# Kernel optimization log

Hardware: AMD Instinct MI355X
Metric: run time of the kernel (lower is better)

The kernel has to match this reference:

```python
import jax, jax.numpy as jnp
import numpy as np

N_NODES = 100000
IN_F = 128
H_F = 128
LOOKBACK = 3
N_EDGES = 640000


def setup_inputs() -> dict:
    key = jax.random.key(0)
    ks = jax.random.split(key, 16)
    s = lambda k, shp: jax.random.normal(k, shp, dtype=jnp.float32) * 0.05
    inp = {
        "feat": jax.random.normal(ks[0], (N_NODES, IN_F), dtype=jnp.float32),
        "edges": jax.random.randint(ks[1], (LOOKBACK, 2, N_EDGES), 0, N_NODES, dtype=jnp.int32),
        # conv1 (SAGEConv pool, in->h) params
        "Wp1": s(ks[2], (IN_F, IN_F)), "bp1": jnp.zeros((IN_F,), jnp.float32),
        "Ws1": s(ks[3], (H_F, IN_F)), "Wn1": s(ks[4], (H_F, IN_F)), "b1": jnp.zeros((H_F,), jnp.float32),
        # BatchNorm1d affine params (training-mode batch stats)
        "gamma": jnp.ones((H_F,), jnp.float32), "beta": jnp.zeros((H_F,), jnp.float32),
        # conv2 (SAGEConv pool, h->h) params
        "Wp2": s(ks[5], (H_F, H_F)), "bp2": jnp.zeros((H_F,), jnp.float32),
        "Ws2": s(ks[6], (H_F, H_F)), "Wn2": s(ks[7], (H_F, H_F)), "b2": jnp.zeros((H_F,), jnp.float32),
    }
    return inp


def _sage_pool_conv(h, src, dst, Wp, bp, Ws, Wn, b):
    # pool aggregator: m = relu(fc_pool(h)); neigh = max over in-edges
    m = jax.nn.relu(h @ Wp.T + bp)                      # [N, d]
    agg = jax.ops.segment_max(m[src], dst, num_segments=N_NODES)  # [N, d]
    agg = jnp.where(jnp.isfinite(agg), agg, 0.0)        # nodes with no in-edges -> 0
    return h @ Ws.T + agg @ Wn.T + b


def _batchnorm(x, gamma, beta, eps=1e-5):
    mu = jnp.mean(x, axis=0)
    var = jnp.var(x, axis=0)
    return (x - mu) * jax.lax.rsqrt(var + eps) * gamma + beta


def reference(feat, edges, Wp1, bp1, Ws1, Wn1, b1, gamma, beta, Wp2, bp2, Ws2, Wn2, b2):
    def per_graph(e):
        src, dst = e[0], e[1]
        h = _sage_pool_conv(feat, src, dst, Wp1, bp1, Ws1, Wn1, b1)
        h = _batchnorm(h, gamma, beta)
        h = jax.nn.relu(h)
        h = _sage_pool_conv(h, src, dst, Wp2, bp2, Ws2, Wn2, b2)
        return h

    return jax.vmap(per_graph)(edges)  # [lookback, N, H_F]
```

## Files before the change

### kernel.cpp

```cpp
#include <hip/hip_runtime.h>
#include <hip/hip_bf16.h>

#define NNODES 100000
#define FD 128
#define NEDGES 640000
#define NB 391
#define NT64 1563
#define GX_TWOA 170
#define GX_ONEW 340
#define GX_HEAD 512
#define OFFS_U32 100032

typedef __bf16 bf16x8 __attribute__((ext_vector_type(8)));
typedef __bf16 bf16x4 __attribute__((ext_vector_type(4)));
typedef float f32x4 __attribute__((ext_vector_type(4)));
typedef unsigned short u16x8 __attribute__((ext_vector_type(8)));

__device__ __forceinline__ bf16x8 cvt8(float4 a, float4 b) {
  bf16x8 r;
  r[0] = (__bf16)a.x; r[1] = (__bf16)a.y; r[2] = (__bf16)a.z; r[3] = (__bf16)a.w;
  r[4] = (__bf16)b.x; r[5] = (__bf16)b.y; r[6] = (__bf16)b.z; r[7] = (__bf16)b.w;
  return r;
}

__device__ __forceinline__ void gl16(const void* g, void* l) {
  __builtin_amdgcn_global_load_lds(
      (const __attribute__((address_space(1))) unsigned int*)g,
      (__attribute__((address_space(3))) unsigned int*)l, 16, 0, 0);
}

__device__ __forceinline__ void stage_abf(const __bf16* A, long row0, int M,
                                          char* l, int wid, int lane) {
  long row = row0 + lane;
  if (row > M - 1) row = M - 1;
  const char* base = (const char*)(A + row * FD);
#pragma unroll
  for (int i = 0; i < 2; ++i) {
    const int s = wid * 2 + i;
    gl16(base + s * 16, l + s * 1024);
  }
}

__device__ __forceinline__ void stage_a32(const float* A, long row0, int M,
                                          char* l, int wid, int lane) {
  long row = row0 + lane;
  if (row > M - 1) row = M - 1;
  const char* base = (const char*)(A + row * FD);
#pragma unroll
  for (int i = 0; i < 4; ++i) {
    const int s = wid * 4 + i;
    gl16(base + s * 16, l + s * 1024);
  }
}

__global__ __launch_bounds__(256) void packw6_k(
    const float* __restrict__ W0, const float* __restrict__ W1,
    const float* __restrict__ W2, const float* __restrict__ W3,
    const float* __restrict__ W4, const float* __restrict__ W5,
    __bf16* __restrict__ out) {
  const int gidx = blockIdx.x * 256 + threadIdx.x;
  const int wi = gidx >> 11;
  const int f = gidx & 2047;
  const float* W = wi == 0 ? W0 : wi == 1 ? W1 : wi == 2 ? W2
                 : wi == 3 ? W3 : wi == 4 ? W4 : W5;
  const int c = f >> 8, kk = (f >> 6) & 3, lane = f & 63;
  const int lr = lane & 15, lg = lane >> 4;
  const float* p = W + (c * 16 + lr) * FD + kk * 32 + lg * 8;
  *(bf16x8*)(out + (long)gidx * 8) = cvt8(*(const float4*)p, *(const float4*)(p + 4));
}

template <int AM>
__device__ __forceinline__ void lds_arow(const char* l, int rl, int lg,
                                         const float* __restrict__ scsh,
                                         bf16x8 (&af)[4]) {
#pragma unroll
  for (int kk = 0; kk < 4; ++kk) {
    if constexpr (AM == 0) {
      const int s = kk * 8 + lg * 2;
      const float4 x = *(const float4*)(l + s * 1024 + rl * 16);
      const float4 y = *(const float4*)(l + (s + 1) * 1024 + rl * 16);
      af[kk] = cvt8(x, y);
    } else {
      const bf16x8 r = *(const bf16x8*)(l + (kk * 4 + lg) * 1024 + rl * 16);
      if constexpr (AM == 3) {
        const int k = lg * 8 + kk * 32;
        const float4 scx = *(const float4*)(scsh + k);
        const float4 scy = *(const float4*)(scsh + k + 4);
        const float4 shx = *(const float4*)(scsh + 128 + k);
        const float4 shy = *(const float4*)(scsh + 128 + k + 4);
        bf16x8 o;
        o[0] = (__bf16)fmaxf((float)r[0] * scx.x + shx.x, 0.f);
        o[1] = (__bf16)fmaxf((float)r[1] * scx.y + shx.y, 0.f);
        o[2] = (__bf16)fmaxf((float)r[2] * scx.z + shx.z, 0.f);
        o[3] = (__bf16)fmaxf((float)r[3] * scx.w + shx.w, 0.f);
        o[4] = (__bf16)fmaxf((float)r[4] * scy.x + shy.x, 0.f);
        o[5] = (__bf16)fmaxf((float)r[5] * scy.y + shy.y, 0.f);
        o[6] = (__bf16)fmaxf((float)r[6] * scy.z + shy.z, 0.f);
        o[7] = (__bf16)fmaxf((float)r[7] * scy.w + shy.w, 0.f);
        af[kk] = o;
      } else {
        af[kk] = r;
      }
    }
  }
}

template <int A0M, int A1M, bool TWOA, bool RELU, bool OUTBF16, bool STATS, bool WRITEB>
__global__ __launch_bounds__(512, 2) void gemm_k(
    const void* __restrict__ A0, long a0s, const void* __restrict__ A1, long a1s,
    const __bf16* __restrict__ W0p, const __bf16* __restrict__ W1p,
    const float* __restrict__ bias, const float* __restrict__ scsh0,
    void* __restrict__ outp, long os, float* __restrict__ pblk,
    __bf16* __restrict__ bcopy, int M) {
  constexpr int ASZ = (A0M == 0) ? 32768 : 16384;
  constexpr int A1SZ = TWOA ? 16384 : 0;
  constexpr int LSZ = 2 * (ASZ + A1SZ) + (STATS ? 2048 : 0);
  __shared__ __align__(16) char lds[LSZ];
  char* lA0a = lds;
  char* lA1a = lds + ASZ;
  char* lA0b = lds + ASZ + A1SZ;
  char* lA1b = lds + 2 * ASZ + A1SZ;
  float* s_red = (float*)(lds + 2 * (ASZ + A1SZ));

  const int g = blockIdx.y;
  const int tid = threadIdx.x;
  const int wid = tid >> 6;
  const int lane = tid & 63;
  const int rw = wid & 1;
  const int cw = wid >> 1;
  const int lr = lane & 15;
  const int lg = lane >> 4;
  const int S = gridDim.x;

  const void* A0g = (const char*)A0 + (long)g * a0s;
  const void* A1g = (const char*)A1 + (TWOA ? (long)g * a1s : 0);
  void* outg = (char*)outp + (long)g * os;
  const float* scshg = (A0M == 3 || A1M == 3) ? scsh0 + (long)g * 256 : nullptr;

  bf16x8 bw0[2][4], bw1[2][4];
#pragma unroll
  for (int ci = 0; ci < 2; ++ci)
#pragma unroll
    for (int kk = 0; kk < 4; ++kk) {
      const long f = ((long)((cw * 2 + ci) * 4 + kk) * 64 + lane) * 8;
      bw0[ci][kk] = *(const bf16x8*)(W0p + f);
      if constexpr (TWOA) bw1[ci][kk] = *(const bf16x8*)(W1p + f);
    }

  float ps[2][4], pss[2][4];
  if constexpr (STATS) {
#pragma unroll
    for (int ci = 0; ci < 2; ++ci)
#pragma unroll
      for (int j = 0; j < 4; ++j) { ps[ci][j] = 0.f; pss[ci][j] = 0.f; }
  }

  auto stageA = [&](long t, char* la0, char* la1) {
    if constexpr (A0M == 0) stage_a32((const float*)A0g, t * 64, M, la0, wid, lane);
    else stage_abf((const __bf16*)A0g, t * 64, M, la0, wid, lane);
    if constexpr (TWOA) stage_abf((const __bf16*)A1g, t * 64, M, la1, wid, lane);
  };

  auto body = [&](long t, long tn, char* la0, char* la1, char* na0, char* na1) {
    if (tn < NT64) stageA(tn, na0, na1);

    bf16x8 a0f[2][4];
#pragma unroll
    for (int tt = 0; tt < 2; ++tt)
      lds_arow<A0M>(la0, rw * 32 + tt * 16 + lr, lg, scshg, a0f[tt]);
    bf16x8 a1f[2][4];
    if constexpr (TWOA) {
#pragma unroll
      for (int tt = 0; tt < 2; ++tt)
        lds_arow<A1M>(la1, rw * 32 + tt * 16 + lr, lg, scshg, a1f[tt]);
    }

    if constexpr (WRITEB) {
      if (cw == 0) {
#pragma unroll
        for (int tt = 0; tt < 2; ++tt) {
          const long row = t * 64 + rw * 32 + tt * 16 + lr;
          if (row < M)
#pragma unroll
            for (int kk = 0; kk < 4; ++kk)
              *(bf16x8*)(bcopy + row * FD + lg * 8 + kk * 32) = a0f[tt][kk];
        }
      }
    }

    f32x4 acc[2][2];
#pragma unroll
    for (int tt = 0; tt < 2; ++tt)
#pragma unroll
      for (int ci = 0; ci < 2; ++ci) acc[tt][ci] = (f32x4){0.f, 0.f, 0.f, 0.f};

#pragma unroll
    for (int ci = 0; ci < 2; ++ci)
#pragma unroll
      for (int tt = 0; tt < 2; ++tt)
#pragma unroll
        for (int kk = 0; kk < 4; ++kk)
          acc[tt][ci] = __builtin_amdgcn_mfma_f32_16x16x32_bf16(bw0[ci][kk], a0f[tt][kk], acc[tt][ci], 0, 0, 0);
    if constexpr (TWOA) {
#pragma unroll
      for (int ci = 0; ci < 2; ++ci)
#pragma unroll
        for (int tt = 0; tt < 2; ++tt)
#pragma unroll
          for (int kk = 0; kk < 4; ++kk)
            acc[tt][ci] = __builtin_amdgcn_mfma_f32_16x16x32_bf16(bw1[ci][kk], a1f[tt][kk], acc[tt][ci], 0, 0, 0);
    }

#pragma unroll
    for (int tt = 0; tt < 2; ++tt) {
      const long row = t * 64 + rw * 32 + tt * 16 + lr;
      const bool ok = row < M;
#pragma unroll
      for (int ci = 0; ci < 2; ++ci) {
        const int cb = cw * 32 + ci * 16 + lg * 4;
        f32x4 v = acc[tt][ci];
        if (bias) {
          const float4 bv = *(const float4*)(bias + cb);
          v[0] += bv.x; v[1] += bv.y; v[2] += bv.z; v[3] += bv.w;
        }
        if constexpr (STATS) {
          if (ok) {
#pragma unroll
            for (int j = 0; j < 4; ++j) { ps[ci][j] += v[j]; pss[ci][j] += v[j] * v[j]; }
          }
        }
        if constexpr (RELU) {
#pragma unroll
          for (int j = 0; j < 4; ++j) v[j] = fmaxf(v[j], 0.f);
        }
        if (ok) {
          if constexpr (OUTBF16) {
            bf16x4 o;
            o[0] = (__bf16)v[0]; o[1] = (__bf16)v[1];
            o[2] = (__bf16)v[2]; o[3] = (__bf16)v[3];
            *(bf16x4*)((__bf16*)outg + row * FD + cb) = o;
          } else {
            *(f32x4*)((float*)outg + row * FD + cb) = v;
          }
        }
      }
    }
    __syncthreads();
  };

  long t = blockIdx.x;
  stageA(t, lA0a, lA1a);
  __syncthreads();

  for (;;) {
    long tn = t + S;
    body(t, tn, lA0a, lA1a, lA0b, lA1b);
    t = tn;
    if (t >= NT64) break;
    tn = t + S;
    body(t, tn, lA0b, lA1b, lA0a, lA1a);
    t = tn;
    if (t >= NT64) break;
  }

  if constexpr (STATS) {
#pragma unroll
    for (int ci = 0; ci < 2; ++ci)
#pragma unroll
      for (int j = 0; j < 4; ++j) {
        float s = ps[ci][j], q = pss[ci][j];
        s += __shfl_xor(s, 1); s += __shfl_xor(s, 2);
        s += __shfl_xor(s, 4); s += __shfl_xor(s, 8);
        q += __shfl_xor(q, 1); q += __shfl_xor(q, 2);
        q += __shfl_xor(q, 4); q += __shfl_xor(q, 8);
        if (lr == 0) {
          s_red[(0 * 8 + wid) * 32 + ci * 16 + lg * 4 + j] = s;
          s_red[(1 * 8 + wid) * 32 + ci * 16 + lg * 4 + j] = q;
        }
      }
    __syncthreads();
    if (tid < 256) {
      const int which = tid >> 7, col = tid & 127;
      const int cwi = col >> 5, cl = col & 31;
      const float a = s_red[(which * 8 + cwi * 2 + 0) * 32 + cl] +
                      s_red[(which * 8 + cwi * 2 + 1) * 32 + cl];
      pblk[((long)g * gridDim.x + blockIdx.x) * 256 + tid] = a;
    }
  }
}

__global__ __launch_bounds__(256) void bn_final2_k(const float* __restrict__ pblk,
                                                   const float* __restrict__ gamma,
                                                   const float* __restrict__ beta,
                                                   float* __restrict__ scsh3) {
  __shared__ float s_ss[128];
  const int g = blockIdx.y;
  const int tid = threadIdx.x;
  const float* p = pblk + (long)g * GX_TWOA * 256;
  float s = 0.f;
  for (int r = 0; r < GX_TWOA; ++r) s += p[r * 256 + tid];
  if (tid >= 128) s_ss[tid - 128] = s;
  __syncthreads();
  if (tid < 128) {
    const float mu = s / (float)NNODES;
    const float var = s_ss[tid] / (float)NNODES - mu * mu;
    const float sc = rsqrtf(var + 1e-5f) * gamma[tid];
    scsh3[g * 256 + tid] = sc;
    scsh3[g * 256 + 128 + tid] = beta[tid] - mu * sc;
  }
}


__global__ __launch_bounds__(256) void hist_rank3_k(const int* __restrict__ edges,
                                                    unsigned* __restrict__ deg3,
                                                    unsigned short* __restrict__ rank3) {
  const int g = blockIdx.y;
  const int e = blockIdx.x * 256 + threadIdx.x;
  if (e < NEDGES) {
    const int d = edges[(long)g * 2 * NEDGES + NEDGES + e];
    const unsigned r = atomicAdd(&deg3[(long)g * NNODES + d], 1u);
    rank3[(long)g * NEDGES + e] = (unsigned short)r;
  }
}

__global__ __launch_bounds__(256) void blocksum3_k(const unsigned* __restrict__ deg3,
                                                   unsigned* __restrict__ bsum3) {
  __shared__ unsigned s[256];
  const int g = blockIdx.y;
  const int i = blockIdx.x * 256 + threadIdx.x;
  s[threadIdx.x] = (i < NNODES) ? deg3[(long)g * NNODES + i] : 0u;
  __syncthreads();
#pragma unroll
  for (int o = 128; o > 0; o >>= 1) {
    if (threadIdx.x < o) s[threadIdx.x] += s[threadIdx.x + o];
    __syncthreads();
  }
  if (threadIdx.x == 0) bsum3[g * NB + blockIdx.x] = s[0];
}

__global__ __launch_bounds__(512) void scanb3_k(const unsigned* __restrict__ bsum3,
                                                unsigned* __restrict__ boffs3,
                                                unsigned* __restrict__ offs3) {
  __shared__ unsigned s[512];
  const int g = blockIdx.y;
  const unsigned v = (threadIdx.x < NB) ? bsum3[g * NB + threadIdx.x] : 0u;
  s[threadIdx.x] = v;
  __syncthreads();
#pragma unroll
  for (int o = 1; o < 512; o <<= 1) {
    unsigned t = (threadIdx.x >= o) ? s[threadIdx.x - o] : 0u;
    __syncthreads();
    s[threadIdx.x] += t;
    __syncthreads();
  }
  if (threadIdx.x < NB) boffs3[g * NB + threadIdx.x] = s[threadIdx.x] - v;
  if (threadIdx.x == 0) offs3[(long)g * OFFS_U32 + NNODES] = NEDGES;
}

__global__ __launch_bounds__(256) void offsets3_k(const unsigned* __restrict__ deg3,
                                                  const unsigned* __restrict__ boffs3,
                                                  unsigned* __restrict__ offs3) {
  __shared__ unsigned s[256];
  const int g = blockIdx.y;
  const int i = blockIdx.x * 256 + threadIdx.x;
  const unsigned v = (i < NNODES) ? deg3[(long)g * NNODES + i] : 0u;
  s[threadIdx.x] = v;
  __syncthreads();
#pragma unroll
  for (int o = 1; o < 256; o <<= 1) {
    unsigned t = (threadIdx.x >= o) ? s[threadIdx.x - o] : 0u;
    __syncthreads();
    s[threadIdx.x] += t;
    __syncthreads();
  }
  const unsigned excl = s[threadIdx.x] - v + boffs3[g * NB + blockIdx.x];
  if (i < NNODES) offs3[(long)g * OFFS_U32 + i] = excl;
}

__global__ __launch_bounds__(256) void scat3_k(const int* __restrict__ edges,
                                               const unsigned* __restrict__ offs3,
                                               const unsigned short* __restrict__ rank3,
                                               int* __restrict__ ssrc3) {
  const int g = blockIdx.y;
  const int e = blockIdx.x * 256 + threadIdx.x;
  if (e < NEDGES) {
    const int s = edges[(long)g * 2 * NEDGES + e];
    const int d = edges[(long)g * 2 * NEDGES + NEDGES + e];
    const unsigned p = offs3[(long)g * OFFS_U32 + d] + rank3[(long)g * NEDGES + e];
    ssrc3[(long)g * NEDGES + p] = s;
  }
}

__global__ __launch_bounds__(256) void agg_k(const unsigned short* __restrict__ m,
                                             long ms, const int* __restrict__ ssrc3,
                                             const unsigned* __restrict__ offs3,
                                             unsigned short* __restrict__ agg3) {
  const int g = blockIdx.y;
  const unsigned short* mg = m + (long)g * ms;
  const int* ssrc = ssrc3 + (long)g * NEDGES;
  const unsigned* offs = offs3 + (long)g * OFFS_U32;
  unsigned short* agg = agg3 + (long)g * NNODES * FD;

  const int gid = blockIdx.x * 256 + threadIdx.x;
  const int node = gid >> 4;
  if (node >= NNODES) return;
  const int fl = (gid & 15) * 8;
  const unsigned beg = offs[node], end = offs[node + 1];
  u16x8 acc = {0, 0, 0, 0, 0, 0, 0, 0};
  unsigned i = beg;
  for (; i + 2 <= end; i += 2) {
    const int s0 = ssrc[i];
    const int s1 = ssrc[i + 1];
    const u16x8 v0 = *(const u16x8*)(mg + (long)s0 * FD + fl);
    const u16x8 v1 = *(const u16x8*)(mg + (long)s1 * FD + fl);
#pragma unroll
    for (int j = 0; j < 8; ++j) {
      const unsigned short mx = v0[j] > v1[j] ? v0[j] : v1[j];
      acc[j] = mx > acc[j] ? mx : acc[j];
    }
  }
  if (i < end) {
    const u16x8 v = *(const u16x8*)(mg + (long)ssrc[i] * FD + fl);
#pragma unroll
    for (int j = 0; j < 8; ++j) acc[j] = v[j] > acc[j] ? v[j] : acc[j];
  }
  *(u16x8*)(agg + (long)node * FD + fl) = acc;
}

__global__ __launch_bounds__(256) void zero_k(float4* __restrict__ p, long n4) {
  const long i = (long)blockIdx.x * 256 + threadIdx.x;
  if (i < n4) p[i] = (float4){0.f, 0.f, 0.f, 0.f};
}

extern "C" void kernel_launch(void* const* d_in, const int* in_sizes, int n_in,
                              void* d_out, int out_size, void* d_ws, size_t ws_size,
                              hipStream_t stream) {
  const float* feat = (const float*)d_in[0];
  const int* edges = (const int*)d_in[1];
  const float* Wp1 = (const float*)d_in[2];
  const float* bp1 = (const float*)d_in[3];
  const float* Ws1 = (const float*)d_in[4];
  const float* Wn1 = (const float*)d_in[5];
  const float* b1 = (const float*)d_in[6];
  const float* gamma = (const float*)d_in[7];
  const float* beta = (const float*)d_in[8];
  const float* Wp2 = (const float*)d_in[9];
  const float* bp2 = (const float*)d_in[10];
  const float* Ws2 = (const float*)d_in[11];
  const float* Wn2 = (const float*)d_in[12];
  const float* b2 = (const float*)d_in[13];

  const long SZ_BF = 25600000;
  const long SZ_F32 = 51200000;

  char* w = (char*)d_ws;
  __bf16* m1 = (__bf16*)w;
  __bf16* featb = (__bf16*)(w + 25600000);
  __bf16* h1b3 = (__bf16*)(w + 51200000);
  __bf16* aggb3 = (__bf16*)(w + 128000000);
  __bf16* m2_3 = (__bf16*)(w + 204800000);
  float* pblk3 = (float*)(w + 204800000);
  __bf16* wpk = (__bf16*)(w + 281600000);
  float* scsh3 = (float*)(w + 281796608);
  unsigned* deg3 = (unsigned*)(w + 281799680);
  unsigned* offs3 = (unsigned*)(w + 282999680);
  unsigned* bsum3 = (unsigned*)(w + 284200064);
  unsigned* boffs3 = (unsigned*)(w + 284204928);
  unsigned short* rank3 = (unsigned short*)(w + 284209792);
  int* ssrc3 = (int*)(w + 288049792);

  __bf16* Wp1p = wpk;
  __bf16* Ws1p = wpk + 16384;
  __bf16* Wn1p = wpk + 2 * 16384;
  __bf16* Wp2p = wpk + 3 * 16384;
  __bf16* Ws2p = wpk + 4 * 16384;
  __bf16* Wn2p = wpk + 5 * 16384;

  const dim3 blk(256);
  const dim3 blk512(512);
  const int edgeGrid = (NEDGES + 255) / 256;
  const int aggGrid = (NNODES * 16 + 255) / 256;
  const int degZeroGrid = (3 * NNODES / 4 + 255) / 256;

  packw6_k<<<48, blk, 0, stream>>>(Wp1, Ws1, Wn1, Wp2, Ws2, Wn2, wpk);

  zero_k<<<degZeroGrid, blk, 0, stream>>>((float4*)deg3, 3L * NNODES / 4);
  hist_rank3_k<<<dim3(edgeGrid, 3), blk, 0, stream>>>(edges, deg3, rank3);
  blocksum3_k<<<dim3(NB, 3), blk, 0, stream>>>(deg3, bsum3);
  scanb3_k<<<dim3(1, 3), dim3(512), 0, stream>>>(bsum3, boffs3, offs3);
  offsets3_k<<<dim3(NB, 3), blk, 0, stream>>>(deg3, boffs3, offs3);
  scat3_k<<<dim3(edgeGrid, 3), blk, 0, stream>>>(edges, offs3, rank3, ssrc3);

  gemm_k<0, 0, false, true, true, false, true><<<dim3(GX_HEAD, 1), blk512, 0, stream>>>(
      feat, 0, nullptr, 0, Wp1p, nullptr, bp1, nullptr, m1, 0, nullptr, featb, NNODES);

  agg_k<<<dim3(aggGrid, 3), blk, 0, stream>>>((const unsigned short*)m1, 0L,
                                              ssrc3, offs3, (unsigned short*)aggb3);
  gemm_k<1, 1, true, false, true, true, false><<<dim3(GX_TWOA, 3), blk512, 0, stream>>>(
      aggb3, SZ_BF, featb, 0, Wn1p, Ws1p, b1, nullptr, h1b3, SZ_BF, pblk3, nullptr, NNODES);
  bn_final2_k<<<dim3(1, 3), blk, 0, stream>>>(pblk3, gamma, beta, scsh3);

  gemm_k<3, 0, false, true, true, false, false><<<dim3(GX_ONEW, 3), blk512, 0, stream>>>(
      h1b3, SZ_BF, nullptr, 0, Wp2p, nullptr, bp2, scsh3, m2_3, SZ_BF, nullptr, nullptr, NNODES);
  agg_k<<<dim3(aggGrid, 3), blk, 0, stream>>>((const unsigned short*)m2_3,
                                              (long)NNODES * FD, ssrc3, offs3,
                                              (unsigned short*)aggb3);
  gemm_k<3, 1, true, false, false, false, false><<<dim3(GX_TWOA, 3), blk512, 0, stream>>>(
      h1b3, SZ_BF, aggb3, SZ_BF, Ws2p, Wn2p, b2, scsh3, d_out, SZ_F32, nullptr, nullptr, NNODES);
}
```

Before: 529.9 us.

## Triple-buffer GEMM A-tile staging with explicit vmcnt waits, halve grid

Replaces the double-buffered LDS staging in the GEMM kernel with a three-buffer ring. The end-of-iteration __syncthreads is swapped for a partial s_waitcnt vmcnt plus a raw s_barrier, so the next tile's async global-to-LDS loads can stay in flight while the current tile is consumed. The grid sizes are halved and launch bounds move to one block per CU to fit the larger LDS footprint. This trades occupancy for deeper prefetch. The hand-coded vmcnt counts must match the actual load counts, including the output stores, or there is a risk of reading stale LDS data.

```diff
diff --git a/kernel.cpp b/kernel.cpp
--- a/kernel.cpp
+++ b/kernel.cpp
@@ -6,9 +6,9 @@
 #define NEDGES 640000
 #define NB 391
 #define NT64 1563
-#define GX_TWOA 170
-#define GX_ONEW 340
-#define GX_HEAD 512
+#define GX_TWOA 85
+#define GX_ONEW 170
+#define GX_HEAD 256
 #define OFFS_U32 100032
 
 typedef __bf16 bf16x8 __attribute__((ext_vector_type(8)));
@@ -21,6 +21,15 @@
   r[0] = (__bf16)a.x; r[1] = (__bf16)a.y; r[2] = (__bf16)a.z; r[3] = (__bf16)a.w;
   r[4] = (__bf16)b.x; r[5] = (__bf16)b.y; r[6] = (__bf16)b.z; r[7] = (__bf16)b.w;
   return r;
+}
+
+template <int N>
+__device__ __forceinline__ void wait_vm() {
+  if constexpr (N == 0) asm volatile("s_waitcnt vmcnt(0)" ::: "memory");
+  else if constexpr (N == 4) asm volatile("s_waitcnt vmcnt(4)" ::: "memory");
+  else if constexpr (N == 6) asm volatile("s_waitcnt vmcnt(6)" ::: "memory");
+  else if constexpr (N == 8) asm volatile("s_waitcnt vmcnt(8)" ::: "memory");
+  else static_assert(N == 0, "unsupported vmcnt");
 }
 
 __device__ __forceinline__ void gl16(const void* g, void* l) {
@@ -106,7 +115,7 @@
 }
 
 template <int A0M, int A1M, bool TWOA, bool RELU, bool OUTBF16, bool STATS, bool WRITEB>
-__global__ __launch_bounds__(512, 2) void gemm_k(
+__global__ __launch_bounds__(512, 1) void gemm_k(
     const void* __restrict__ A0, long a0s, const void* __restrict__ A1, long a1s,
     const __bf16* __restrict__ W0p, const __bf16* __restrict__ W1p,
     const float* __restrict__ bias, const float* __restrict__ scsh0,
@@ -114,13 +123,12 @@
     __bf16* __restrict__ bcopy, int M) {
   constexpr int ASZ = (A0M == 0) ? 32768 : 16384;
   constexpr int A1SZ = TWOA ? 16384 : 0;
-  constexpr int LSZ = 2 * (ASZ + A1SZ) + (STATS ? 2048 : 0);
+  constexpr int BSZ = ASZ + A1SZ;
+  constexpr int LSZ = 3 * BSZ + (STATS ? 2048 : 0);
+  constexpr int G = (A0M == 0 ? 4 : 2) + (TWOA ? 2 : 0);
+  constexpr int KMAIN = G + 4;
   __shared__ __align__(16) char lds[LSZ];
-  char* lA0a = lds;
-  char* lA1a = lds + ASZ;
-  char* lA0b = lds + ASZ + A1SZ;
-  char* lA1b = lds + 2 * ASZ + A1SZ;
-  float* s_red = (float*)(lds + 2 * (ASZ + A1SZ));
+  float* s_red = (float*)(lds + 3 * BSZ);
 
   const int g = blockIdx.y;
   const int tid = threadIdx.x;
@@ -155,24 +163,31 @@
       for (int j = 0; j < 4; ++j) { ps[ci][j] = 0.f; pss[ci][j] = 0.f; }
   }
 
-  auto stageA = [&](long t, char* la0, char* la1) {
-    if constexpr (A0M == 0) stage_a32((const float*)A0g, t * 64, M, la0, wid, lane);
-    else stage_abf((const __bf16*)A0g, t * 64, M, la0, wid, lane);
-    if constexpr (TWOA) stage_abf((const __bf16*)A1g, t * 64, M, la1, wid, lane);
+  auto stageA = [&](long t, char* buf) {
+    if constexpr (A0M == 0) stage_a32((const float*)A0g, t * 64, M, buf, wid, lane);
+    else stage_abf((const __bf16*)A0g, t * 64, M, buf, wid, lane);
+    if constexpr (TWOA) stage_abf((const __bf16*)A1g, t * 64, M, buf + ASZ, wid, lane);
   };
 
-  auto body = [&](long t, long tn, char* la0, char* la1, char* na0, char* na1) {
-    if (tn < NT64) stageA(tn, na0, na1);
+  auto body = [&](long t, long tn, char* cur, char* nxt) {
+    if (tn < NT64) {
+      stageA(tn, nxt);
+      wait_vm<KMAIN>();
+    } else {
+      wait_vm<4>();
+    }
+    __builtin_amdgcn_s_barrier();
+    __builtin_amdgcn_sched_barrier(0);
 
     bf16x8 a0f[2][4];
 #pragma unroll
     for (int tt = 0; tt < 2; ++tt)
-      lds_arow<A0M>(la0, rw * 32 + tt * 16 + lr, lg, scshg, a0f[tt]);
+      lds_arow<A0M>(cur, rw * 32 + tt * 16 + lr, lg, scshg, a0f[tt]);
     bf16x8 a1f[2][4];
     if constexpr (TWOA) {
 #pragma unroll
       for (int tt = 0; tt < 2; ++tt)
-        lds_arow<A1M>(la1, rw * 32 + tt * 16 + lr, lg, scshg, a1f[tt]);
+        lds_arow<A1M>(cur + ASZ, rw * 32 + tt * 16 + lr, lg, scshg, a1f[tt]);
     }
 
     if constexpr (WRITEB) {
@@ -245,20 +260,23 @@
         }
       }
     }
-    __syncthreads();
   };
 
   long t = blockIdx.x;
-  stageA(t, lA0a, lA1a);
+  stageA(t, lds);
   __syncthreads();
 
   for (;;) {
     long tn = t + S;
-    body(t, tn, lA0a, lA1a, lA0b, lA1b);
+    body(t, tn, lds, lds + BSZ);
     t = tn;
     if (t >= NT64) break;
     tn = t + S;
-    body(t, tn, lA0b, lA1b, lA0a, lA1a);
+    body(t, tn, lds + BSZ, lds + 2 * BSZ);
+    t = tn;
+    if (t >= NT64) break;
+    tn = t + S;
+    body(t, tn, lds + 2 * BSZ, lds);
     t = tn;
     if (t >= NT64) break;
   }
```

Measured after the change: 529.8 us. Within noise of the previous version (-0.0%).
